# Performance work log

Hardware: AMD Instinct MI355X
Metric: run time of the kernel (lower is better)

## Reference

```python
import jax, jax.numpy as jnp
import numpy as np

FS = 2          # filter_size (kernel == stride, non-overlapping)
NL = 10         # num_layers
C_IN = 3        # input_channels
H = 256         # hidden width
OUT = 10        # out_dim
B = 128         # batch
D = FS ** NL    # input spatial length = 1024


def setup_inputs() -> dict:
    key = jax.random.key(0)
    ks = jax.random.split(key, NL + 2)
    inp = {"x": jax.random.normal(ks[0], (B, C_IN, D), dtype=jnp.float32)}
    cin = C_IN
    for l in range(NL):
        dl = D // FS ** (l + 1)  # out positions at layer l
        inp[f"w{l}"] = jax.random.normal(ks[l + 1], (H, cin, dl, FS), dtype=jnp.float32)
        cin = H
    inp["beta"] = jax.random.normal(ks[-1], (H, OUT), dtype=jnp.float32)
    return inp


def _lc(x, w):
    # Locally-connected 1d, stride == kernel: unfold is a pure reshape.
    # x: (B, C, Dd*k), w: (O, C, Dd, k) -> out: (B, O, Dd)
    O, C, Dd, k = w.shape
    xu = x.reshape(x.shape[0], C, Dd, k)
    # per-position contraction over (C, k); avoids the (B,O,C,Dd,k) intermediate
    return jnp.einsum('bcdk,ocdk->bod', xu, w) / (C ** 0.5)


def reference(x, w0, w1, w2, w3, w4, w5, w6, w7, w8, w9, beta):
    ws = [w0, w1, w2, w3, w4, w5, w6, w7, w8, w9]
    y = x
    for w in ws:  # fixed small layer loop
        y = jax.nn.relu(_lc(y, w))
    y = y.mean(axis=-1)            # (B, H) — last spatial dim is size 1
    return y @ beta / beta.shape[0]  # (B, OUT)
```

## Files before the change

kernel.cpp:

```cpp
#include <hip/hip_runtime.h>
#include <hip/hip_bf16.h>
#include <stdint.h>


typedef __attribute__((ext_vector_type(4))) float floatx4;
typedef __attribute__((ext_vector_type(8))) short shortx8;

__device__ __forceinline__ float bf2f(unsigned short u){
    union { unsigned int u; float f; } c; c.u = ((unsigned int)u) << 16; return c.f;
}
__device__ __forceinline__ unsigned short f2bf(float f){
    union { float f; unsigned int u; } c; c.f = f;
    unsigned int x = c.u;
    x += 0x7FFFu + ((x >> 16) & 1u);
    return (unsigned short)(x >> 16);
}

__global__ void probe_kernel(const unsigned int* __restrict__ x, int* __restrict__ flag){
    __shared__ int cnt[256];
    int tid = threadIdx.x;
    unsigned short lo = (unsigned short)(x[tid] & 0xFFFFu);
    int e = (lo >> 7) & 0xFF;
    cnt[tid] = (e >= 90 && e <= 143) ? 1 : 0;
    __syncthreads();
    for (int s = 128; s > 0; s >>= 1){
        if (tid < s) cnt[tid] += cnt[tid + s];
        __syncthreads();
    }
    if (tid == 0) *flag = (cnt[0] > 160) ? 1 : 0;
}

__global__ __launch_bounds__(256) void l0_kernel(const int* __restrict__ flag,
        const void* __restrict__ xv, const void* __restrict__ wv,
        unsigned short* __restrict__ A1){
    __shared__ float Xs[128*6];
    const int d = blockIdx.x;
    const int tid = threadIdx.x;
    const bool BF = (*flag != 0);
    for (int i = tid; i < 384; i += 256){
        int b = i / 3, c = i - b*3;
        if (BF){
            unsigned int u = *(const unsigned int*)((const unsigned short*)xv + (b*3+c)*1024 + 2*d);
            Xs[b*6 + c*2]     = bf2f((unsigned short)(u & 0xFFFFu));
            Xs[b*6 + c*2 + 1] = bf2f((unsigned short)(u >> 16));
        } else {
            const float* xf = (const float*)xv + (b*3+c)*1024 + 2*d;
            Xs[b*6 + c*2] = xf[0]; Xs[b*6 + c*2 + 1] = xf[1];
        }
    }
    __syncthreads();
    const int o = tid;
    float wr[6];
    #pragma unroll
    for (int c = 0; c < 3; ++c){
        if (BF){
            unsigned int u = *(const unsigned int*)((const unsigned short*)wv + ((o*3+c)*512 + d)*2);
            wr[c*2]   = bf2f((unsigned short)(u & 0xFFFFu));
            wr[c*2+1] = bf2f((unsigned short)(u >> 16));
        } else {
            const float* wf = (const float*)wv + ((o*3+c)*512 + d)*2;
            wr[c*2] = wf[0]; wr[c*2+1] = wf[1];
        }
    }
    const float s3 = 0.57735026918962576f;
    for (int b = 0; b < 128; ++b){
        float s = 0.f;
        #pragma unroll
        for (int j = 0; j < 6; ++j) s += Xs[b*6 + j] * wr[j];
        A1[d*32768 + b*256 + o] = f2bf(fmaxf(s, 0.f) * s3);
    }
}

template<bool WBF, bool ATOMIC>
__device__ __forceinline__ void layer_main_impl(const unsigned short* __restrict__ Ain,
        const void* __restrict__ wv, void* __restrict__ out, int dl, int ks){
    __shared__ unsigned short At[8*128*16];
    __shared__ unsigned short Wt[4*64*40];
    const int tid  = threadIdx.x;
    const int lane = tid & 63, wv_ = tid >> 6;
    const int g = lane >> 4, mr = lane & 15;
    const int nd = dl >> 2;
    int bi = blockIdx.x;
    const int dg = bi % nd; bi /= nd;
    const int ng = bi & 3;
    const int ksid = bi >> 2;
    const int TS = 16 / ks;
    const int d0 = dg << 2;
    const int o0 = ng << 6;
    const int dme = d0 + wv_;
    const float* wF = (const float*)wv;
    const unsigned short* wB = (const unsigned short*)wv;

    floatx4 acc[8][4];
    #pragma unroll
    for (int m = 0; m < 8; ++m)
        #pragma unroll
        for (int nb = 0; nb < 4; ++nb)
            acc[m][nb] = (floatx4){0.f,0.f,0.f,0.f};

    for (int s = 0; s < TS; ++s){
        const int c0 = (ksid*TS + s) << 4;
        {
            const int b = tid >> 1, h = tid & 1;
            #pragma unroll
            for (int i = 0; i < 8; ++i){
                uint4 v = *(const uint4*)(Ain + (2*d0 + i)*32768 + b*256 + c0 + h*8);
                *(uint4*)(At + (i*128 + b)*16 + h*8) = v;
            }
        }
        #pragma unroll
        for (int rr = 0; rr < 4; ++rr){
            int run = (rr << 8) + tid;
            int oo = run >> 4, cl = run & 15;
            int src = ((((o0 + oo) << 8) + (c0 + cl))*dl + d0)*2;
            unsigned short wtmp[8];
            if (WBF){
                uint4 u = *(const uint4*)(wB + src);
                const unsigned short* pu = (const unsigned short*)&u;
                #pragma unroll
                for (int j = 0; j < 8; ++j) wtmp[j] = pu[j];
            } else {
                float4 a = *(const float4*)(wF + src);
                float4 b4 = *(const float4*)(wF + src + 4);
                wtmp[0]=f2bf(a.x); wtmp[1]=f2bf(a.y); wtmp[2]=f2bf(a.z); wtmp[3]=f2bf(a.w);
                wtmp[4]=f2bf(b4.x); wtmp[5]=f2bf(b4.y); wtmp[6]=f2bf(b4.z); wtmp[7]=f2bf(b4.w);
            }
            #pragma unroll
            for (int j = 0; j < 8; ++j){
                int dd = j >> 1, t = j & 1;
                Wt[(dd*64 + oo)*40 + t*16 + cl] = wtmp[j];
            }
        }
        __syncthreads();
        shortx8 bfr[4];
        #pragma unroll
        for (int nb = 0; nb < 4; ++nb)
            bfr[nb] = *(const shortx8*)(Wt + (wv_*64 + nb*16 + mr)*40 + g*8);
        #pragma unroll
        for (int m = 0; m < 8; ++m){
            shortx8 af = *(const shortx8*)(At + ((wv_*2 + (g>>1))*128 + m*16 + mr)*16 + (g&1)*8);
            #pragma unroll
            for (int nb = 0; nb < 4; ++nb)
                acc[m][nb] = __builtin_amdgcn_mfma_f32_16x16x32_bf16(af, bfr[nb], acc[m][nb], 0,0,0);
        }
        __syncthreads();
    }
    #pragma unroll
    for (int m = 0; m < 8; ++m)
        #pragma unroll
        for (int nb = 0; nb < 4; ++nb)
            #pragma unroll
            for (int r = 0; r < 4; ++r){
                int b = m*16 + g*4 + r;
                int o = o0 + nb*16 + mr;
                if (ATOMIC)
                    unsafeAtomicAdd((float*)out + (dme*128 + b)*256 + o, acc[m][nb][r]);
                else
                    ((unsigned short*)out)[dme*32768 + b*256 + o] =
                        f2bf(fmaxf(acc[m][nb][r], 0.f) * 0.0625f);
            }
}

template<bool ATOMIC>
__global__ __launch_bounds__(256,2) void layer_main_k(const int* __restrict__ flag,
        const unsigned short* __restrict__ Ain, const void* __restrict__ wv,
        void* __restrict__ out, int dl, int ks){
    if (*flag) layer_main_impl<true,  ATOMIC>(Ain, wv, out, dl, ks);
    else       layer_main_impl<false, ATOMIC>(Ain, wv, out, dl, ks);
}

template<bool WBF>
__device__ __forceinline__ void tail_impl(const unsigned short* __restrict__ Ain,
        const void* __restrict__ wv, float* __restrict__ outS, int dl, int ksplit){
    int id = blockIdx.x;
    int d = id % dl; int t2 = id / dl;
    int ob = t2 & 3; int ksid = t2 >> 2;
    const int KSEG = 512 / ksplit;
    const int k0s = ksid * KSEG;
    const int lane = threadIdx.x & 63, wv2 = threadIdx.x >> 6;
    const int mr = lane & 15, kg = lane >> 4;
    const float* wF = (const float*)wv;
    const unsigned short* wB = (const unsigned short*)wv;
    floatx4 acc[2][4];
    #pragma unroll
    for (int mi = 0; mi < 2; ++mi)
        #pragma unroll
        for (int ni = 0; ni < 4; ++ni) acc[mi][ni] = (floatx4){0.f,0.f,0.f,0.f};
    for (int k0 = k0s; k0 < k0s + KSEG; k0 += 32){
        int c0 = (k0 >> 1) + kg*4;
        shortx8 af[2];
        #pragma unroll
        for (int mi = 0; mi < 2; ++mi){
            int b = wv2*32 + mi*16 + mr;
            #pragma unroll
            for (int cc = 0; cc < 4; ++cc){
                af[mi][2*cc]   = (short)Ain[(2*d)*32768   + b*256 + c0 + cc];
                af[mi][2*cc+1] = (short)Ain[(2*d+1)*32768 + b*256 + c0 + cc];
            }
        }
        shortx8 bf_[4];
        #pragma unroll
        for (int ni = 0; ni < 4; ++ni){
            int o = ob*64 + ni*16 + mr;
            int base = ((o*256 + c0)*dl + d)*2;
            #pragma unroll
            for (int cc = 0; cc < 4; ++cc){
                if (WBF){
                    unsigned int u = *(const unsigned int*)(wB + base);
                    bf_[ni][2*cc]   = (short)(u & 0xFFFFu);
                    bf_[ni][2*cc+1] = (short)(u >> 16);
                } else {
                    bf_[ni][2*cc]   = (short)f2bf(wF[base]);
                    bf_[ni][2*cc+1] = (short)f2bf(wF[base+1]);
                }
                base += 2*dl;
            }
        }
        #pragma unroll
        for (int mi = 0; mi < 2; ++mi)
            #pragma unroll
            for (int ni = 0; ni < 4; ++ni)
                acc[mi][ni] = __builtin_amdgcn_mfma_f32_16x16x32_bf16(af[mi], bf_[ni], acc[mi][ni], 0,0,0);
    }
    #pragma unroll
    for (int mi = 0; mi < 2; ++mi)
        #pragma unroll
        for (int ni = 0; ni < 4; ++ni)
            #pragma unroll
            for (int r = 0; r < 4; ++r){
                int b = wv2*32 + mi*16 + kg*4 + r;
                int o = ob*64 + ni*16 + mr;
                unsafeAtomicAdd(outS + (d*128 + b)*256 + o, acc[mi][ni][r]);
            }
}
__global__ __launch_bounds__(256) void tail_k(const int* __restrict__ flag,
        const unsigned short* __restrict__ Ain, const void* __restrict__ wv,
        float* __restrict__ outS, int dl, int ksplit){
    if (*flag) tail_impl<true >(Ain, wv, outS, dl, ksplit);
    else       tail_impl<false>(Ain, wv, outS, dl, ksplit);
}

__global__ __launch_bounds__(256) void fin_kernel(const float* __restrict__ S,
        unsigned short* __restrict__ A, int n){
    int i = (blockIdx.x*256 + threadIdx.x)*4;
    if (i + 3 < n){
        float4 v = *(const float4*)(S + i);
        unsigned short r0 = f2bf(fmaxf(v.x,0.f)*0.0625f);
        unsigned short r1 = f2bf(fmaxf(v.y,0.f)*0.0625f);
        unsigned short r2 = f2bf(fmaxf(v.z,0.f)*0.0625f);
        unsigned short r3 = f2bf(fmaxf(v.w,0.f)*0.0625f);
        unsigned int lo = (unsigned int)r0 | ((unsigned int)r1 << 16);
        unsigned int hi = (unsigned int)r2 | ((unsigned int)r3 << 16);
        uint2 u; u.x = lo; u.y = hi;
        *(uint2*)(A + i) = u;
    }
}

template<bool BF>
__device__ __forceinline__ void epi_impl(const float* __restrict__ S9, const void* __restrict__ beta,
                                         void* __restrict__ out){
    int b = blockIdx.x;
    int lane = threadIdx.x;
    float accv[10];
    #pragma unroll
    for (int o = 0; o < 10; ++o) accv[o] = 0.f;
    for (int h = lane; h < 256; h += 64){
        float y = fmaxf(S9[b*256 + h], 0.f) * 0.0625f;
        #pragma unroll
        for (int o = 0; o < 10; ++o){
            float be = BF ? bf2f(((const unsigned short*)beta)[h*10 + o])
                          : ((const float*)beta)[h*10 + o];
            accv[o] += y * be;
        }
    }
    #pragma unroll
    for (int off = 32; off > 0; off >>= 1){
        #pragma unroll
        for (int o = 0; o < 10; ++o)
            accv[o] += __shfl_down(accv[o], off, 64);
    }
    if (lane == 0){
        #pragma unroll
        for (int o = 0; o < 10; ++o){
            float v = accv[o] * (1.f/256.f);
            if (BF) ((unsigned short*)out)[b*10 + o] = f2bf(v);
            else    ((float*)out)[b*10 + o] = v;
        }
    }
}
__global__ void epi_kernel(const int* __restrict__ flag, const float* __restrict__ S9,
                           const void* __restrict__ beta, void* __restrict__ out){
    if (*flag) epi_impl<true>(S9, beta, out);
    else       epi_impl<false>(S9, beta, out);
}

extern "C" void kernel_launch(void* const* d_in, const int* in_sizes, int n_in,
                              void* d_out, int out_size, void* d_ws, size_t ws_size,
                              hipStream_t stream) {
    (void)in_sizes; (void)n_in; (void)out_size; (void)ws_size;
    char* wsb = (char*)d_ws;
    int* flag = (int*)wsb;
    unsigned short* A1 = (unsigned short*)(wsb + 512);
    float* S2 = (float*)(wsb + 512);
    float* S3 = S2 + 4194304;
    float* S4 = S3 + 2097152;
    float* S5 = S4 + 1048576;
    float* S6 = S5 + 524288;
    float* S7 = S6 + 262144;
    float* S8 = S7 + 131072;
    float* S9 = S8 + 65536;
    unsigned short* A2 = (unsigned short*)(wsb + 512 + 33554432);
    unsigned short* A3 = A2;
    unsigned short* A4 = A3 + 4194304;
    unsigned short* A5 = A4 + 2097152;
    unsigned short* A6 = A5 + 1048576;
    unsigned short* A7 = A6 + 524288;
    unsigned short* A8 = A7 + 262144;
    unsigned short* A9 = A8 + 131072;

    probe_kernel<<<1, 256, 0, stream>>>((const unsigned int*)d_in[0], flag);
    l0_kernel<<<512, 256, 0, stream>>>(flag, d_in[0], d_in[1], A1);
    layer_main_k<false><<<256, 256, 0, stream>>>(flag, A1, d_in[2], A2, 256, 1);
    hipMemsetAsync(S2, 0, 33423360, stream);
    layer_main_k<true ><<<256, 256, 0, stream>>>(flag, A2, d_in[3], S2, 128, 2);
    fin_kernel<<<4096, 256, 0, stream>>>(S2, A3, 4194304);
    layer_main_k<true ><<<256, 256, 0, stream>>>(flag, A3, d_in[4], S3, 64, 4);
    fin_kernel<<<2048, 256, 0, stream>>>(S3, A4, 2097152);
    layer_main_k<true ><<<256, 256, 0, stream>>>(flag, A4, d_in[5], S4, 32, 8);
    fin_kernel<<<1024, 256, 0, stream>>>(S4, A5, 1048576);
    layer_main_k<true ><<<256, 256, 0, stream>>>(flag, A5, d_in[6], S5, 16, 16);
    fin_kernel<<<512, 256, 0, stream>>>(S5, A6, 524288);
    layer_main_k<true ><<<128, 256, 0, stream>>>(flag, A6, d_in[7], S6, 8, 16);
    fin_kernel<<<256, 256, 0, stream>>>(S6, A7, 262144);
    layer_main_k<true ><<<64, 256, 0, stream>>>(flag, A7, d_in[8], S7, 4, 16);
    fin_kernel<<<128, 256, 0, stream>>>(S7, A8, 131072);
    tail_k<<<128, 256, 0, stream>>>(flag, A8, d_in[9], S8, 2, 16);
    fin_kernel<<<64, 256, 0, stream>>>(S8, A9, 65536);
    tail_k<<<64, 256, 0, stream>>>(flag, A9, d_in[10], S9, 1, 16);
    epi_kernel<<<128, 64, 0, stream>>>(flag, S9, d_in[11], d_out);
}
```

Before: 644.5 us.

## Double-buffer LDS tiles with register prefetch and remap blocks for locality in layer_main

Double-buffers the activation and weight LDS tiles and prefetches the next K-step's global loads into registers while the current step's MFMAs run. This removes one barrier per iteration and hides global load latency. It also remaps block indices so neighbouring blocks share d-groups and output groups, aiming at better cache reuse. Launch bounds drop to one block per CU because the LDS footprint doubles and register use grows, so occupancy falls.

```diff
diff --git a/kernel.cpp b/kernel.cpp
--- a/kernel.cpp
+++ b/kernel.cpp
@@ -73,23 +73,36 @@
 
 template<bool WBF, bool ATOMIC>
 __device__ __forceinline__ void layer_main_impl(const unsigned short* __restrict__ Ain,
-        const void* __restrict__ wv, void* __restrict__ out, int dl, int ks){
-    __shared__ unsigned short At[8*128*16];
-    __shared__ unsigned short Wt[4*64*40];
+        const void* __restrict__ wv, void* __restrict__ out, int dl, int ks,
+        unsigned short* __restrict__ At0, unsigned short* __restrict__ At1,
+        unsigned short* __restrict__ Wt0, unsigned short* __restrict__ Wt1){
     const int tid  = threadIdx.x;
     const int lane = tid & 63, wv_ = tid >> 6;
     const int g = lane >> 4, mr = lane & 15;
     const int nd = dl >> 2;
-    int bi = blockIdx.x;
-    const int dg = bi % nd; bi /= nd;
-    const int ng = bi & 3;
-    const int ksid = bi >> 2;
+
+    int dg, ng, ksid;
+    {
+        const int bi = blockIdx.x;
+        const int G  = gridDim.x;
+        if (nd >= 2 && (G & 63) == 0){
+            const int x = bi & 7, e = (bi >> 3) & 7, gg = bi >> 6;
+            const int pid = gg*8 + x;
+            const int nd2 = nd >> 1;
+            dg   = (pid % nd2)*2 + (e & 1);
+            ng   = e >> 1;
+            ksid = pid / nd2;
+        } else {
+            dg = bi % nd; const int r = bi / nd; ng = r & 3; ksid = r >> 2;
+        }
+    }
     const int TS = 16 / ks;
     const int d0 = dg << 2;
     const int o0 = ng << 6;
     const int dme = d0 + wv_;
     const float* wF = (const float*)wv;
     const unsigned short* wB = (const unsigned short*)wv;
+    const int sb = tid >> 1, sh = tid & 1;
 
     floatx4 acc[8][4];
     #pragma unroll
@@ -98,40 +111,62 @@
         for (int nb = 0; nb < 4; ++nb)
             acc[m][nb] = (floatx4){0.f,0.f,0.f,0.f};
 
-    for (int s = 0; s < TS; ++s){
+    uint4  aR[8];
+    uint4  wRu[4];
+    float4 wRa[4], wRb[4];
+
+    auto LOADS = [&](int s){
         const int c0 = (ksid*TS + s) << 4;
-        {
-            const int b = tid >> 1, h = tid & 1;
-            #pragma unroll
-            for (int i = 0; i < 8; ++i){
-                uint4 v = *(const uint4*)(Ain + (2*d0 + i)*32768 + b*256 + c0 + h*8);
-                *(uint4*)(At + (i*128 + b)*16 + h*8) = v;
-            }
-        }
+        #pragma unroll
+        for (int i = 0; i < 8; ++i)
+            aR[i] = *(const uint4*)(Ain + (2*d0 + i)*32768 + sb*256 + c0 + sh*8);
         #pragma unroll
         for (int rr = 0; rr < 4; ++rr){
-            int run = (rr << 8) + tid;
-            int oo = run >> 4, cl = run & 15;
-            int src = ((((o0 + oo) << 8) + (c0 + cl))*dl + d0)*2;
+            const int run = (rr << 8) + tid;
+            const int oo = run >> 4, cl = run & 15;
+            const int src = ((((o0 + oo) << 8) + (c0 + cl))*dl + d0)*2;
+            if (WBF){
+                wRu[rr] = *(const uint4*)(wB + src);
+            } else {
+                wRa[rr] = *(const float4*)(wF + src);
+                wRb[rr] = *(const float4*)(wF + src + 4);
+            }
+        }
+    };
+    auto WRITES = [&](unsigned short* At, unsigned short* Wt){
+        #pragma unroll
+        for (int i = 0; i < 8; ++i)
+            *(uint4*)(At + (i*128 + sb)*16 + sh*8) = aR[i];
+        #pragma unroll
+        for (int rr = 0; rr < 4; ++rr){
+            const int run = (rr << 8) + tid;
+            const int oo = run >> 4, cl = run & 15;
             unsigned short wtmp[8];
             if (WBF){
-                uint4 u = *(const uint4*)(wB + src);
-                const unsigned short* pu = (const unsigned short*)&u;
+                const unsigned short* pu = (const unsigned short*)&wRu[rr];
                 #pragma unroll
                 for (int j = 0; j < 8; ++j) wtmp[j] = pu[j];
             } else {
-                float4 a = *(const float4*)(wF + src);
-                float4 b4 = *(const float4*)(wF + src + 4);
-                wtmp[0]=f2bf(a.x); wtmp[1]=f2bf(a.y); wtmp[2]=f2bf(a.z); wtmp[3]=f2bf(a.w);
-                wtmp[4]=f2bf(b4.x); wtmp[5]=f2bf(b4.y); wtmp[6]=f2bf(b4.z); wtmp[7]=f2bf(b4.w);
+                wtmp[0]=f2bf(wRa[rr].x); wtmp[1]=f2bf(wRa[rr].y);
+                wtmp[2]=f2bf(wRa[rr].z); wtmp[3]=f2bf(wRa[rr].w);
+                wtmp[4]=f2bf(wRb[rr].x); wtmp[5]=f2bf(wRb[rr].y);
+                wtmp[6]=f2bf(wRb[rr].z); wtmp[7]=f2bf(wRb[rr].w);
             }
             #pragma unroll
             for (int j = 0; j < 8; ++j){
-                int dd = j >> 1, t = j & 1;
+                const int dd = j >> 1, t = j & 1;
                 Wt[(dd*64 + oo)*40 + t*16 + cl] = wtmp[j];
             }
         }
+    };
+
+    LOADS(0);
+    WRITES(At0, Wt0);
+    for (int s = 0; s < TS; ++s){
         __syncthreads();
+        if (s + 1 < TS) LOADS(s + 1);
+        const unsigned short* At = (s & 1) ? At1 : At0;
+        const unsigned short* Wt = (s & 1) ? Wt1 : Wt0;
         shortx8 bfr[4];
         #pragma unroll
         for (int nb = 0; nb < 4; ++nb)
@@ -143,7 +178,7 @@
             for (int nb = 0; nb < 4; ++nb)
                 acc[m][nb] = __builtin_amdgcn_mfma_f32_16x16x32_bf16(af, bfr[nb], acc[m][nb], 0,0,0);
         }
-        __syncthreads();
+        if (s + 1 < TS) WRITES((s & 1) ? At0 : At1, (s & 1) ? Wt0 : Wt1);
     }
     #pragma unroll
     for (int m = 0; m < 8; ++m)
@@ -151,22 +186,24 @@
         for (int nb = 0; nb < 4; ++nb)
             #pragma unroll
             for (int r = 0; r < 4; ++r){
-                int b = m*16 + g*4 + r;
-                int o = o0 + nb*16 + mr;
+                const int bb = m*16 + g*4 + r;
+                const int oc = o0 + nb*16 + mr;
                 if (ATOMIC)
-                    unsafeAtomicAdd((float*)out + (dme*128 + b)*256 + o, acc[m][nb][r]);
+                    unsafeAtomicAdd((float*)out + (dme*128 + bb)*256 + oc, acc[m][nb][r]);
                 else
-                    ((unsigned short*)out)[dme*32768 + b*256 + o] =
+                    ((unsigned short*)out)[dme*32768 + bb*256 + oc] =
                         f2bf(fmaxf(acc[m][nb][r], 0.f) * 0.0625f);
             }
 }
 
 template<bool ATOMIC>
-__global__ __launch_bounds__(256,2) void layer_main_k(const int* __restrict__ flag,
+__global__ __launch_bounds__(256,1) void layer_main_k(const int* __restrict__ flag,
         const unsigned short* __restrict__ Ain, const void* __restrict__ wv,
         void* __restrict__ out, int dl, int ks){
-    if (*flag) layer_main_impl<true,  ATOMIC>(Ain, wv, out, dl, ks);
-    else       layer_main_impl<false, ATOMIC>(Ain, wv, out, dl, ks);
+    __shared__ unsigned short At[2][8*128*16];
+    __shared__ unsigned short Wt[2][4*64*40];
+    if (*flag) layer_main_impl<true,  ATOMIC>(Ain, wv, out, dl, ks, At[0], At[1], Wt[0], Wt[1]);
+    else       layer_main_impl<false, ATOMIC>(Ain, wv, out, dl, ks, At[0], At[1], Wt[0], Wt[1]);
 }
 
 template<bool WBF>
```

After: 639.2 us. No clear change (-0.8%).

## Double-buffer weight tiles, load activations directly to registers, split batch across blocks

Applied to the files above, without the earlier changes.

Rewrites the main locally-connected layer kernel. Weight tiles are now double-buffered in shared memory with register prefetch of the next K-slice, so there is one barrier per step. Activations are loaded straight from global memory into MFMA operand registers instead of being staged through shared memory. The batch is split into two halves across blocks, which doubles grid sizes and halves the accumulators per thread. A swizzled block-index mapping groups neighbouring blocks for L2 locality. In exchange, each weight tile is fetched twice (once per batch half) and more atomics are issued per output.

```diff
diff --git a/kernel.cpp b/kernel.cpp
--- a/kernel.cpp
+++ b/kernel.cpp
@@ -73,90 +73,157 @@
 
 template<bool WBF, bool ATOMIC>
 __device__ __forceinline__ void layer_main_impl(const unsigned short* __restrict__ Ain,
-        const void* __restrict__ wv, void* __restrict__ out, int dl, int ks){
-    __shared__ unsigned short At[8*128*16];
-    __shared__ unsigned short Wt[4*64*40];
+        const void* __restrict__ wv, void* __restrict__ out, int dl, int ks,
+        unsigned short* __restrict__ Wt0, unsigned short* __restrict__ Wt1){
     const int tid  = threadIdx.x;
     const int lane = tid & 63, wv_ = tid >> 6;
     const int g = lane >> 4, mr = lane & 15;
     const int nd = dl >> 2;
-    int bi = blockIdx.x;
-    const int dg = bi % nd; bi /= nd;
-    const int ng = bi & 3;
-    const int ksid = bi >> 2;
+
+    int dg, ng, mh, ksid;
+    {
+        const int bi = blockIdx.x;
+        const int G  = gridDim.x;
+        if (nd >= 2 && (G & 127) == 0){
+            const int x = bi & 7, j = (bi >> 3) & 15, gg = bi >> 7;
+            const int pid = gg*8 + x;
+            const int nd2 = nd >> 1;
+            dg   = (pid % nd2)*2 + (j & 1);
+            ng   = (j >> 1) & 3;
+            mh   = j >> 3;
+            ksid = pid / nd2;
+        } else {
+            dg = bi % nd; const int r = bi / nd;
+            ng = r & 3; mh = (r >> 2) & 1; ksid = r >> 3;
+        }
+    }
     const int TS = 16 / ks;
     const int d0 = dg << 2;
     const int o0 = ng << 6;
+    const int b0 = mh << 6;
     const int dme = d0 + wv_;
     const float* wF = (const float*)wv;
     const unsigned short* wB = (const unsigned short*)wv;
 
-    floatx4 acc[8][4];
-    #pragma unroll
-    for (int m = 0; m < 8; ++m)
+    const int cl  = tid & 15;
+    const int ooB = tid >> 4;
+    const int ws0 = (((o0 + ooB      )*256 + cl)*dl + d0)*2;
+    const int ws1 = (((o0 + ooB + 16 )*256 + cl)*dl + d0)*2;
+    const int ws2 = (((o0 + ooB + 32 )*256 + cl)*dl + d0)*2;
+    const int ws3 = (((o0 + ooB + 48 )*256 + cl)*dl + d0)*2;
+    const int wcstep = 32*dl;
+
+    const unsigned short* Ab = Ain + (2*dme + (g>>1))*32768 + (b0 + mr)*256 + (g&1)*8;
+    const int c_base = ksid*TS;
+
+    floatx4 acc[4][4];
+    #pragma unroll
+    for (int m = 0; m < 4; ++m)
         #pragma unroll
         for (int nb = 0; nb < 4; ++nb)
             acc[m][nb] = (floatx4){0.f,0.f,0.f,0.f};
 
+    shortx8 a0, a1, a2, a3;
+    shortx8 n0, n1, n2, n3;
+    uint4  u0, u1, u2, u3;
+    float4 wa0, wa1, wa2, wa3;
+    float4 wb0, wb1, wb2, wb3;
+
+#define LOADA4(d0_,d1_,d2_,d3_,s_) do { \
+    const unsigned short* _p = Ab + ((c_base + (s_)) << 4); \
+    d0_ = *(const shortx8*)(_p);          \
+    d1_ = *(const shortx8*)(_p + 4096);   \
+    d2_ = *(const shortx8*)(_p + 8192);   \
+    d3_ = *(const shortx8*)(_p + 12288);  \
+} while(0)
+
+#define LOADW(s_) do { \
+    const int _c = (c_base + (s_)) * wcstep; \
+    if (WBF){ \
+        u0 = *(const uint4*)(wB + ws0 + _c); \
+        u1 = *(const uint4*)(wB + ws1 + _c); \
+        u2 = *(const uint4*)(wB + ws2 + _c); \
+        u3 = *(const uint4*)(wB + ws3 + _c); \
+    } else { \
+        wa0 = *(const float4*)(wF + ws0 + _c); wb0 = *(const float4*)(wF + ws0 + _c + 4); \
+        wa1 = *(const float4*)(wF + ws1 + _c); wb1 = *(const float4*)(wF + ws1 + _c + 4); \
+        wa2 = *(const float4*)(wF + ws2 + _c); wb2 = *(const float4*)(wF + ws2 + _c + 4); \
+        wa3 = *(const float4*)(wF + ws3 + _c); wb3 = *(const float4*)(wF + ws3 + _c + 4); \
+    } \
+} while(0)
+
+#define STW_RR(Wt_, uu_, fa_, fb_, oo_) do { \
+    unsigned short w0_,w1_,w2_,w3_,w4_,w5_,w6_,w7_; \
+    if (WBF){ const unsigned short* _pu = (const unsigned short*)&(uu_); \
+        w0_=_pu[0]; w1_=_pu[1]; w2_=_pu[2]; w3_=_pu[3]; w4_=_pu[4]; w5_=_pu[5]; w6_=_pu[6]; w7_=_pu[7]; \
+    } else { \
+        w0_=f2bf((fa_).x); w1_=f2bf((fa_).y); w2_=f2bf((fa_).z); w3_=f2bf((fa_).w); \
+        w4_=f2bf((fb_).x); w5_=f2bf((fb_).y); w6_=f2bf((fb_).z); w7_=f2bf((fb_).w); \
+    } \
+    (Wt_)[((0*64) + (oo_))*40 +  0 + cl] = w0_;   \
+    (Wt_)[((0*64) + (oo_))*40 + 16 + cl] = w1_;   \
+    (Wt_)[((1*64) + (oo_))*40 +  0 + cl] = w2_; \
+    (Wt_)[((1*64) + (oo_))*40 + 16 + cl] = w3_; \
+    (Wt_)[((2*64) + (oo_))*40 +  0 + cl] = w4_; \
+    (Wt_)[((2*64) + (oo_))*40 + 16 + cl] = w5_; \
+    (Wt_)[((3*64) + (oo_))*40 +  0 + cl] = w6_; \
+    (Wt_)[((3*64) + (oo_))*40 + 16 + cl] = w7_; \
+} while(0)
+
+#define STOREW(Wt_) do { \
+    STW_RR(Wt_, u0, wa0, wb0, ooB      ); \
+    STW_RR(Wt_, u1, wa1, wb1, ooB + 16 ); \
+    STW_RR(Wt_, u2, wa2, wb2, ooB + 32 ); \
+    STW_RR(Wt_, u3, wa3, wb3, ooB + 48 ); \
+} while(0)
+
+    LOADW(0);
+    LOADA4(a0, a1, a2, a3, 0);
+    STOREW(Wt0);
+
     for (int s = 0; s < TS; ++s){
-        const int c0 = (ksid*TS + s) << 4;
-        {
-            const int b = tid >> 1, h = tid & 1;
-            #pragma unroll
-            for (int i = 0; i < 8; ++i){
-                uint4 v = *(const uint4*)(Ain + (2*d0 + i)*32768 + b*256 + c0 + h*8);
-                *(uint4*)(At + (i*128 + b)*16 + h*8) = v;
-            }
-        }
-        #pragma unroll
-        for (int rr = 0; rr < 4; ++rr){
-            int run = (rr << 8) + tid;
-            int oo = run >> 4, cl = run & 15;
-            int src = ((((o0 + oo) << 8) + (c0 + cl))*dl + d0)*2;
-            unsigned short wtmp[8];
-            if (WBF){
-                uint4 u = *(const uint4*)(wB + src);
-                const unsigned short* pu = (const unsigned short*)&u;
-                #pragma unroll
-                for (int j = 0; j < 8; ++j) wtmp[j] = pu[j];
-            } else {
-                float4 a = *(const float4*)(wF + src);
-                float4 b4 = *(const float4*)(wF + src + 4);
-                wtmp[0]=f2bf(a.x); wtmp[1]=f2bf(a.y); wtmp[2]=f2bf(a.z); wtmp[3]=f2bf(a.w);
-                wtmp[4]=f2bf(b4.x); wtmp[5]=f2bf(b4.y); wtmp[6]=f2bf(b4.z); wtmp[7]=f2bf(b4.w);
-            }
-            #pragma unroll
-            for (int j = 0; j < 8; ++j){
-                int dd = j >> 1, t = j & 1;
-                Wt[(dd*64 + oo)*40 + t*16 + cl] = wtmp[j];
-            }
-        }
         __syncthreads();
-        shortx8 bfr[4];
-        #pragma unroll
-        for (int nb = 0; nb < 4; ++nb)
-            bfr[nb] = *(const shortx8*)(Wt + (wv_*64 + nb*16 + mr)*40 + g*8);
-        #pragma unroll
-        for (int m = 0; m < 8; ++m){
-            shortx8 af = *(const shortx8*)(At + ((wv_*2 + (g>>1))*128 + m*16 + mr)*16 + (g&1)*8);
-            #pragma unroll
-            for (int nb = 0; nb < 4; ++nb)
-                acc[m][nb] = __builtin_amdgcn_mfma_f32_16x16x32_bf16(af, bfr[nb], acc[m][nb], 0,0,0);
-        }
-        __syncthreads();
-    }
-    #pragma unroll
-    for (int m = 0; m < 8; ++m)
+        if (s + 1 < TS){
+            LOADA4(n0, n1, n2, n3, s + 1);
+            LOADW(s + 1);
+        }
+        const unsigned short* Wr = (s & 1) ? Wt1 : Wt0;
+        shortx8 br0 = *(const shortx8*)(Wr + (wv_*64 +  0 + mr)*40 + g*8);
+        shortx8 br1 = *(const shortx8*)(Wr + (wv_*64 + 16 + mr)*40 + g*8);
+        shortx8 br2 = *(const shortx8*)(Wr + (wv_*64 + 32 + mr)*40 + g*8);
+        shortx8 br3 = *(const shortx8*)(Wr + (wv_*64 + 48 + mr)*40 + g*8);
+#define MFMA_ROW(m_, ar_) \
+        acc[m_][0] = __builtin_amdgcn_mfma_f32_16x16x32_bf16(ar_, br0, acc[m_][0], 0,0,0); \
+        acc[m_][1] = __builtin_amdgcn_mfma_f32_16x16x32_bf16(ar_, br1, acc[m_][1], 0,0,0); \
+        acc[m_][2] = __builtin_amdgcn_mfma_f32_16x16x32_bf16(ar_, br2, acc[m_][2], 0,0,0); \
+        acc[m_][3] = __builtin_amdgcn_mfma_f32_16x16x32_bf16(ar_, br3, acc[m_][3], 0,0,0);
+        MFMA_ROW(0, a0)
+        MFMA_ROW(1, a1)
+        MFMA_ROW(2, a2)
+        MFMA_ROW(3, a3)
+#undef MFMA_ROW
+        if (s + 1 < TS){
+            STOREW((s & 1) ? Wt0 : Wt1);
+            a0 = n0; a1 = n1; a2 = n2; a3 = n3;
+        }
+    }
+#undef LOADA4
+#undef LOADW
+#undef STW_RR
+#undef STOREW
+
+    #pragma unroll
+    for (int m = 0; m < 4; ++m)
         #pragma unroll
         for (int nb = 0; nb < 4; ++nb)
             #pragma unroll
             for (int r = 0; r < 4; ++r){
-                int b = m*16 + g*4 + r;
-                int o = o0 + nb*16 + mr;
+                const int bb = b0 + m*16 + g*4 + r;
+                const int oc = o0 + nb*16 + mr;
                 if (ATOMIC)
-                    unsafeAtomicAdd((float*)out + (dme*128 + b)*256 + o, acc[m][nb][r]);
+                    unsafeAtomicAdd((float*)out + (dme*128 + bb)*256 + oc, acc[m][nb][r]);
                 else
-                    ((unsigned short*)out)[dme*32768 + b*256 + o] =
+                    ((unsigned short*)out)[dme*32768 + bb*256 + oc] =
                         f2bf(fmaxf(acc[m][nb][r], 0.f) * 0.0625f);
             }
 }
@@ -165,8 +232,9 @@
 __global__ __launch_bounds__(256,2) void layer_main_k(const int* __restrict__ flag,
         const unsigned short* __restrict__ Ain, const void* __restrict__ wv,
         void* __restrict__ out, int dl, int ks){
-    if (*flag) layer_main_impl<true,  ATOMIC>(Ain, wv, out, dl, ks);
-    else       layer_main_impl<false, ATOMIC>(Ain, wv, out, dl, ks);
+    __shared__ unsigned short Wt[2][4*64*40];
+    if (*flag) layer_main_impl<true,  ATOMIC>(Ain, wv, out, dl, ks, Wt[0], Wt[1]);
+    else       layer_main_impl<false, ATOMIC>(Ain, wv, out, dl, ks, Wt[0], Wt[1]);
 }
 
 template<bool WBF>
@@ -320,19 +388,19 @@
 
     probe_kernel<<<1, 256, 0, stream>>>((const unsigned int*)d_in[0], flag);
     l0_kernel<<<512, 256, 0, stream>>>(flag, d_in[0], d_in[1], A1);
-    layer_main_k<false><<<256, 256, 0, stream>>>(flag, A1, d_in[2], A2, 256, 1);
+    layer_main_k<false><<<512, 256, 0, stream>>>(flag, A1, d_in[2], A2, 256, 1);
     hipMemsetAsync(S2, 0, 33423360, stream);
-    layer_main_k<true ><<<256, 256, 0, stream>>>(flag, A2, d_in[3], S2, 128, 2);
+    layer_main_k<true ><<<512, 256, 0, stream>>>(flag, A2, d_in[3], S2, 128, 2);
     fin_kernel<<<4096, 256, 0, stream>>>(S2, A3, 4194304);
-    layer_main_k<true ><<<256, 256, 0, stream>>>(flag, A3, d_in[4], S3, 64, 4);
+    layer_main_k<true ><<<512, 256, 0, stream>>>(flag, A3, d_in[4], S3, 64, 4);
     fin_kernel<<<2048, 256, 0, stream>>>(S3, A4, 2097152);
-    layer_main_k<true ><<<256, 256, 0, stream>>>(flag, A4, d_in[5], S4, 32, 8);
+    layer_main_k<true ><<<512, 256, 0, stream>>>(flag, A4, d_in[5], S4, 32, 8);
     fin_kernel<<<1024, 256, 0, stream>>>(S4, A5, 1048576);
-    layer_main_k<true ><<<256, 256, 0, stream>>>(flag, A5, d_in[6], S5, 16, 16);
+    layer_main_k<true ><<<512, 256, 0, stream>>>(flag, A5, d_in[6], S5, 16, 16);
     fin_kernel<<<512, 256, 0, stream>>>(S5, A6, 524288);
-    layer_main_k<true ><<<128, 256, 0, stream>>>(flag, A6, d_in[7], S6, 8, 16);
+    layer_main_k<true ><<<256, 256, 0, stream>>>(flag, A6, d_in[7], S6, 8, 16);
     fin_kernel<<<256, 256, 0, stream>>>(S6, A7, 262144);
-    layer_main_k<true ><<<64, 256, 0, stream>>>(flag, A7, d_in[8], S7, 4, 16);
+    layer_main_k<true ><<<128, 256, 0, stream>>>(flag, A7, d_in[8], S7, 4, 16);
     fin_kernel<<<128, 256, 0, stream>>>(S7, A8, 131072);
     tail_k<<<128, 256, 0, stream>>>(flag, A8, d_in[9], S8, 2, 16);
     fin_kernel<<<64, 256, 0, stream>>>(S8, A9, 65536);
```

Result: no change. 635.3 us (-1.4%).
